# Kernel optimization log

Hardware: AMD Instinct MI355X
Metric: run time of the kernel (lower is better)

The kernel has to match this reference:

```python
import jax, jax.numpy as jnp
import numpy as np

DT = 0.1
TAU_HP = 12.3  # Tm1 high-pass time constant
TAU_LP = 2.3   # Tm1 low-pass time constant

N_NEURONS = 200_000
N_EDGES = 6_400_000
N_TM1 = 25_000
STEPS = 50


def setup_inputs() -> dict:
    key = jax.random.key(0)
    k1, k2, k3, k4 = jax.random.split(key, 4)
    tm1_input = jax.random.normal(k1, (STEPS, N_TM1), dtype=jnp.float32)
    weights = jax.random.normal(k2, (N_EDGES,), dtype=jnp.float32) * 0.1
    tau = jnp.ones((N_NEURONS,), dtype=jnp.float32)      # tau_init = 1.0 per type
    vrest = jnp.zeros((N_NEURONS,), dtype=jnp.float32)   # vrest_init = 0.0 per type
    source_idx = jax.random.randint(k3, (N_EDGES,), 0, N_NEURONS, dtype=jnp.int32)
    target_idx = jax.random.randint(k4, (N_EDGES,), 0, N_NEURONS, dtype=jnp.int32)
    return {
        "tm1_input": tm1_input,
        "weights": weights,
        "tau": tau,
        "vrest": vrest,
        "source_idx": source_idx,
        "target_idx": target_idx,
        "n_tm1": N_TM1,
    }


def reference(tm1_input, weights, tau, vrest, source_idx, target_idx, n_tm1):
    n_neurons = tau.shape[0]

    def step(carry, x):
        v, tm1_f, tm1_v = carry
        # Tm1 temporal filters: high-pass then rectify then low-pass
        hp_out = x - tm1_f                                   # [n_tm1]
        tm1_f_new = tm1_f + DT * (x - tm1_f) / TAU_HP
        rect_out = jax.nn.relu(hp_out)
        # write (old) tm1_v into the Tm1 slice of v before recurrence
        v = v.at[:n_tm1].set(tm1_v)
        tm1_v_new = tm1_v + DT * (rect_out - tm1_v) / TAU_LP
        # gather -> weight -> scatter-add message passing
        r = jax.nn.relu(v)                                   # [n_neurons]
        edge_currents = r[source_idx] * weights              # [n_edges]
        synaptic_input = jax.ops.segment_sum(
            edge_currents, target_idx, num_segments=n_neurons)
        external = jnp.zeros_like(v).at[:n_tm1].set(tm1_v_new)
        dv = (-v + synaptic_input + vrest + external) / tau
        dv = dv.at[:n_tm1].set(0.0)                          # Tm1 driven by its filters
        v = v + DT * dv
        return (v, tm1_f_new, tm1_v_new), None

    v0 = jnp.zeros((tau.shape[0],), dtype=tm1_input.dtype)
    f0 = jnp.zeros((n_tm1,), dtype=tm1_input.dtype)
    tv0 = jnp.zeros((n_tm1,), dtype=tm1_input.dtype)
    (v, _, _), _ = jax.lax.scan(step, (v0, f0, tv0), tm1_input)
    return v[None, :]  # [1, n_neurons], matches torch batch=1
```

## Files before the change

kernel.cpp:

```cpp
#include <hip/hip_runtime.h>
#include <hip/hip_bf16.h>

#define DT 0.1f
#define TAU_HP 12.3f
#define TAU_LP 2.3f
#define SCAN_B 1024

#define BSHIFT 7
#define BMASK 127
#define BMAX 2048
#define CHUNK 32768
#define B4_CAP 6144
#define MWMAX 6400


__global__ void init_kernel(float* __restrict__ vA,
                            float* __restrict__ tm1_f,
                            unsigned* __restrict__ mask3,
                            int n_neurons, int n_tm1, int mask3_words) {
    int i = blockIdx.x * blockDim.x + threadIdx.x;
    if (i < n_neurons) vA[i] = 0.0f;
    if (i < n_tm1) tm1_f[i] = 0.0f;
    if (i < mask3_words) mask3[i] = 0u;
}

__global__ void bhist_kernel(const int* __restrict__ tgt, int* __restrict__ blkhist,
                             int n_edges, int n_tm1, int nb, int nblk) {
    __shared__ int hist[BMAX];
    int b = blockIdx.x;
    for (int i = threadIdx.x; i < nb; i += blockDim.x) hist[i] = 0;
    __syncthreads();
    int base = b * CHUNK;
    int end = min(base + CHUNK, n_edges);
    for (int k = base + threadIdx.x; k < end; k += blockDim.x) {
        int t = tgt[k];
        if (t >= n_tm1) atomicAdd(&hist[t >> BSHIFT], 1);
    }
    __syncthreads();
    for (int i = threadIdx.x; i < nb; i += blockDim.x)
        blkhist[(size_t)i * nblk + b] = hist[i];
}

__global__ void scan1_kernel(const int* in, int* out, int* bsums, int n) {
    __shared__ int s[SCAN_B];
    int gid = blockIdx.x * SCAN_B + threadIdx.x;
    int x = (gid < n) ? in[gid] : 0;
    s[threadIdx.x] = x;
    __syncthreads();
    for (int off = 1; off < SCAN_B; off <<= 1) {
        int t = (threadIdx.x >= off) ? s[threadIdx.x - off] : 0;
        __syncthreads();
        s[threadIdx.x] += t;
        __syncthreads();
    }
    if (gid < n) out[gid] = s[threadIdx.x] - x;
    if (threadIdx.x == SCAN_B - 1) bsums[blockIdx.x] = s[SCAN_B - 1];
}

__global__ void scan2_kernel(int* bsums, int nb, int* total) {
    __shared__ int s[SCAN_B];
    int x = (threadIdx.x < nb) ? bsums[threadIdx.x] : 0;
    s[threadIdx.x] = x;
    __syncthreads();
    for (int off = 1; off < SCAN_B; off <<= 1) {
        int t = (threadIdx.x >= off) ? s[threadIdx.x - off] : 0;
        __syncthreads();
        s[threadIdx.x] += t;
        __syncthreads();
    }
    if (threadIdx.x == nb - 1) *total = s[threadIdx.x];
    if (threadIdx.x < nb) bsums[threadIdx.x] = s[threadIdx.x] - x;
}

__global__ void scanadd_kernel(int* data, const int* __restrict__ bsums, int n) {
    int gid = blockIdx.x * blockDim.x + threadIdx.x;
    if (gid < n) data[gid] += bsums[gid / SCAN_B];
}

__global__ void bin_kernel(const int* __restrict__ src, const int* __restrict__ tgt,
                           const float* __restrict__ w, const int* __restrict__ scanned,
                           int2* __restrict__ edges, int n_edges, int n_tm1,
                           int nb, int nblk) {
    __shared__ int cur[BMAX];
    int b = blockIdx.x;
    for (int i = threadIdx.x; i < nb; i += blockDim.x)
        cur[i] = scanned[(size_t)i * nblk + b];
    __syncthreads();
    int base = b * CHUNK;
    int end = min(base + CHUNK, n_edges);
    for (int k = base + threadIdx.x; k < end; k += blockDim.x) {
        int t = tgt[k];
        if (t < n_tm1) continue;
        int pos = atomicAdd(&cur[t >> BSHIFT], 1);
        edges[pos] = make_int2(src[k] | ((t & BMASK) << 18), __float_as_int(w[k]));
    }
}

__global__ void finalize_kernel(int2* edges, const int* __restrict__ scanned,
                                int* __restrict__ row_start,
                                const int* __restrict__ total,
                                int n_neurons, int nb, int nblk) {
    __shared__ int2 buf[B4_CAP];
    __shared__ int hist[BMASK + 1], ls[BMASK + 1], cur[BMASK + 1];
    int b = blockIdx.x;
    int n_kept = *total;
    int beg = scanned[(size_t)b * nblk];
    int end = (b == nb - 1) ? n_kept : scanned[(size_t)(b + 1) * nblk];
    int n = min(end - beg, B4_CAP);

    for (int k = threadIdx.x; k < n; k += blockDim.x) buf[k] = edges[beg + k];
    if (threadIdx.x <= BMASK) hist[threadIdx.x] = 0;
    __syncthreads();
    for (int k = threadIdx.x; k < n; k += blockDim.x)
        atomicAdd(&hist[(buf[k].x >> 18) & BMASK], 1);
    __syncthreads();
    if (threadIdx.x <= BMASK) ls[threadIdx.x] = hist[threadIdx.x];
    __syncthreads();
    for (int off = 1; off <= BMASK; off <<= 1) {
        int t = (threadIdx.x <= BMASK && threadIdx.x >= off) ? ls[threadIdx.x - off] : 0;
        __syncthreads();
        if (threadIdx.x <= BMASK) ls[threadIdx.x] += t;
        __syncthreads();
    }
    if (threadIdx.x <= BMASK) {
        int excl = ls[threadIdx.x] - hist[threadIdx.x];
        cur[threadIdx.x] = excl;
        int t = (b << BSHIFT) + threadIdx.x;
        if (t < n_neurons) row_start[t] = beg + excl;
    }
    if (b == nb - 1 && threadIdx.x == 0) row_start[n_neurons] = n_kept;
    __syncthreads();
    for (int k = threadIdx.x; k < n; k += blockDim.x) {
        int2 r = buf[k];
        int pos = atomicAdd(&cur[(r.x >> 18) & BMASK], 1);
        edges[beg + pos] = make_int2(r.x & 0x3FFFF, r.y);
    }
}

__global__ __launch_bounds__(1024)
void step_kernel(const int* __restrict__ row_start,
                 const int2* __restrict__ edges,
                 const float* __restrict__ vr,
                 float* __restrict__ vw,
                 float* __restrict__ tm1_f,
                 const float* __restrict__ x,
                 const float* __restrict__ tau,
                 const float* __restrict__ vrest,
                 const unsigned* __restrict__ maskR,
                 unsigned* __restrict__ maskW,
                 unsigned* __restrict__ maskC,
                 int mask_words,
                 int n_neurons, int n_tm1, int gbase, int last) {
    __shared__ unsigned smask[MWMAX];
    int g = blockIdx.x * blockDim.x + threadIdx.x;

    if ((int)((blockIdx.x + 1) * blockDim.x) > gbase) {
        for (int i = threadIdx.x; i < mask_words; i += blockDim.x)
            smask[i] = maskR[i];
        __syncthreads();
    }

    if (g < gbase) {
        if (g < mask_words) maskC[g] = 0u;
        float val = 0.0f;
        bool wrote = false;
        if (g < n_tm1) {
            float cur = vr[g];
            if (last) {
                val = cur;
            } else {
                float f  = tm1_f[g];
                float xk = x[g];
                float hp = xk - f;
                tm1_f[g] = f + DT * (xk - f) / TAU_HP;
                val = cur + DT * (fmaxf(hp, 0.0f) - cur) / TAU_LP;
            }
            vw[g] = val;
            wrote = true;
        }
        unsigned long long bm = __ballot(wrote && (val > 0.0f));
        int l = threadIdx.x & 63;
        unsigned lo = (unsigned)(bm & 0xffffffffull);
        unsigned hi = (unsigned)(bm >> 32);
        if (l == 0 && lo)  atomicOr(&maskW[g >> 5], lo);
        if (l == 32 && hi) atomicOr(&maskW[g >> 5], hi);
        return;
    }

    int t = g - gbase;
    int row = n_tm1 + (t >> 3);
    int lane = t & 7;
    bool active = (row < n_neurons);
    float sum = 0.0f;
    float vnew = 0.0f;

    if (active) {
        int s = row_start[row];
        int e = row_start[row + 1];
        for (int p = (s & ~1) + 2 * lane; p < e; p += 16) {
            int4 q = *(const int4*)(edges + p);
            bool a0 = (p >= s)    && ((smask[(unsigned)q.x >> 5] >> (q.x & 31)) & 1u);
            bool a1 = (p + 1 < e) && ((smask[(unsigned)q.z >> 5] >> (q.z & 31)) & 1u);
            if (a0) sum += vr[q.x] * __int_as_float(q.y);
            if (a1) sum += vr[q.z] * __int_as_float(q.w);
        }
    }
    sum += __shfl_xor(sum, 4);
    sum += __shfl_xor(sum, 2);
    sum += __shfl_xor(sum, 1);
    if (active && lane == 0) {
        float vi = vr[row];
        vnew = vi + DT * ((-vi + sum + vrest[row]) / tau[row]);
        vw[row] = vnew;
    }
    unsigned long long bm = __ballot(active && lane == 0 && vnew > 0.0f);
    if ((threadIdx.x & 63) == 0) {
        unsigned b8 = 0;
        #pragma unroll
        for (int i = 0; i < 8; ++i) b8 |= (unsigned)((bm >> (8 * i)) & 1ull) << i;
        if (b8) {
            int row0 = n_tm1 + (t >> 3);
            atomicOr(&maskW[row0 >> 5], b8 << (row0 & 31));
        }
    }
}

extern "C" void kernel_launch(void* const* d_in, const int* in_sizes, int n_in,
                              void* d_out, int out_size, void* d_ws, size_t ws_size,
                              hipStream_t stream) {
    const float* tm1_input  = (const float*)d_in[0];
    const float* weights    = (const float*)d_in[1];
    const float* tau        = (const float*)d_in[2];
    const float* vrest      = (const float*)d_in[3];
    const int*   source_idx = (const int*)d_in[4];
    const int*   target_idx = (const int*)d_in[5];

    const int n_edges   = in_sizes[1];
    const int n_neurons = in_sizes[2];
    const int n_tm1     = 25000;
    const int steps     = in_sizes[0] / n_tm1;

    const int nb   = (n_neurons + BMASK) >> BSHIFT;
    const int nblk = (n_edges + CHUNK - 1) / CHUNK;
    const int n_scan = nb * nblk;
    const int mask_words = (n_neurons + 31) >> 5;

    size_t off = 0;
    auto alloc = [&](size_t n) { size_t o = off; off += n; return o; };
    int* ws_i = (int*)d_ws;
    float* ws_f = (float*)d_ws;

    int2*     edges     = (int2*)(ws_i + alloc((size_t)(n_edges + 2) * 2));
    float*    vA        = ws_f + alloc(n_neurons);
    float*    vB        = ws_f + alloc(n_neurons);
    float*    tm1_f     = ws_f + alloc(n_tm1);
    int*      row_start = ws_i + alloc(n_neurons + 1);
    unsigned* mask3     = (unsigned*)(ws_i + alloc((size_t)3 * mask_words));
    int*      blkhist   = ws_i + alloc((size_t)n_scan);
    int*      bsums     = ws_i + alloc(SCAN_B);
    int*      total     = ws_i + alloc(1);
    (void)ws_size;

    float* out = (float*)d_out;

    const int B = 256;
    const int gridN = (n_neurons + B - 1) / B;
    const int nScanBlocks = (n_scan + SCAN_B - 1) / SCAN_B;
    const int gridSA = (n_scan + B - 1) / B;

    const int SB = 1024;
    const int gbase = (n_tm1 + 63) & ~63;
    const int work  = gbase + (n_neurons - n_tm1) * 8;
    const int gridG = (work + SB - 1) / SB;

    init_kernel<<<gridN, B, 0, stream>>>(vA, tm1_f, mask3, n_neurons, n_tm1,
                                         3 * mask_words);
    bhist_kernel<<<nblk, 1024, 0, stream>>>(target_idx, blkhist, n_edges, n_tm1,
                                            nb, nblk);
    scan1_kernel<<<nScanBlocks, SCAN_B, 0, stream>>>(blkhist, blkhist, bsums, n_scan);
    scan2_kernel<<<1, SCAN_B, 0, stream>>>(bsums, nScanBlocks, total);
    scanadd_kernel<<<gridSA, B, 0, stream>>>(blkhist, bsums, n_scan);
    bin_kernel<<<nblk, 1024, 0, stream>>>(source_idx, target_idx, weights, blkhist,
                                          edges, n_edges, n_tm1, nb, nblk);
    finalize_kernel<<<nb, 1024, 0, stream>>>(edges, blkhist, row_start, total,
                                             n_neurons, nb, nblk);

    for (int k = 0; k < steps; ++k) {
        const float* vr = (k & 1) ? vB : vA;
        float* vw = (k == steps - 1) ? out : ((k & 1) ? vA : vB);
        unsigned* mW = mask3 + (size_t)(k % 3) * mask_words;
        unsigned* mR = mask3 + (size_t)((k + 2) % 3) * mask_words;
        unsigned* mC = mask3 + (size_t)((k + 1) % 3) * mask_words;
        step_kernel<<<gridG, SB, 0, stream>>>(
            row_start, edges, vr, vw, tm1_f,
            tm1_input + (size_t)k * n_tm1,
            tau, vrest, mR, mW, mC, mask_words,
            n_neurons, n_tm1, gbase, (k == steps - 1) ? 1 : 0);
    }
}
```

Baseline: 1.779 ms.

## Build CSR with global per-target histogram and atomic scatter

Replaces the two-level bucketed CSR build (block histograms, bucket scatter, then an in-shared-memory per-bucket sort) with a direct global atomic histogram over target neurons, a scan, and a global atomic scatter into per-row cursors. This drops the blkhist matrix and the finalize pass, cutting preprocessing kernels and memory traffic. In exchange it relies on contended global atomics and scattered writes. Edge order within a row becomes nondeterministic, so the floating-point summation order varies between runs.

```diff
diff --git a/kernel.cpp b/kernel.cpp
--- a/kernel.cpp
+++ b/kernel.cpp
@@ -5,40 +5,28 @@
 #define TAU_HP 12.3f
 #define TAU_LP 2.3f
 #define SCAN_B 1024
-
-#define BSHIFT 7
-#define BMASK 127
-#define BMAX 2048
-#define CHUNK 32768
-#define B4_CAP 6144
 #define MWMAX 6400
 
 
 __global__ void init_kernel(float* __restrict__ vA,
                             float* __restrict__ tm1_f,
                             unsigned* __restrict__ mask3,
+                            int* __restrict__ row_start,
                             int n_neurons, int n_tm1, int mask3_words) {
     int i = blockIdx.x * blockDim.x + threadIdx.x;
     if (i < n_neurons) vA[i] = 0.0f;
     if (i < n_tm1) tm1_f[i] = 0.0f;
     if (i < mask3_words) mask3[i] = 0u;
-}
-
-__global__ void bhist_kernel(const int* __restrict__ tgt, int* __restrict__ blkhist,
-                             int n_edges, int n_tm1, int nb, int nblk) {
-    __shared__ int hist[BMAX];
-    int b = blockIdx.x;
-    for (int i = threadIdx.x; i < nb; i += blockDim.x) hist[i] = 0;
-    __syncthreads();
-    int base = b * CHUNK;
-    int end = min(base + CHUNK, n_edges);
-    for (int k = base + threadIdx.x; k < end; k += blockDim.x) {
-        int t = tgt[k];
-        if (t >= n_tm1) atomicAdd(&hist[t >> BSHIFT], 1);
-    }
-    __syncthreads();
-    for (int i = threadIdx.x; i < nb; i += blockDim.x)
-        blkhist[(size_t)i * nblk + b] = hist[i];
+    if (i <= n_neurons) row_start[i] = 0;
+}
+
+__global__ void ghist_kernel(const int* __restrict__ tgt, int* __restrict__ hist,
+                             int n_edges, int n_tm1) {
+    int stride = gridDim.x * blockDim.x;
+    for (int i = blockIdx.x * blockDim.x + threadIdx.x; i < n_edges; i += stride) {
+        int t = tgt[i];
+        if (t >= n_tm1) atomicAdd(&hist[t], 1);
+    }
 }
 
 __global__ void scan1_kernel(const int* in, int* out, int* bsums, int n) {
@@ -77,63 +65,27 @@
     if (gid < n) data[gid] += bsums[gid / SCAN_B];
 }
 
-__global__ void bin_kernel(const int* __restrict__ src, const int* __restrict__ tgt,
-                           const float* __restrict__ w, const int* __restrict__ scanned,
-                           int2* __restrict__ edges, int n_edges, int n_tm1,
-                           int nb, int nblk) {
-    __shared__ int cur[BMAX];
-    int b = blockIdx.x;
-    for (int i = threadIdx.x; i < nb; i += blockDim.x)
-        cur[i] = scanned[(size_t)i * nblk + b];
-    __syncthreads();
-    int base = b * CHUNK;
-    int end = min(base + CHUNK, n_edges);
-    for (int k = base + threadIdx.x; k < end; k += blockDim.x) {
-        int t = tgt[k];
+__global__ void mkcur_kernel(const int* __restrict__ row_start,
+                             int* __restrict__ cur,
+                             int* __restrict__ rs_tail,
+                             const int* __restrict__ total, int n_neurons) {
+    int i = blockIdx.x * blockDim.x + threadIdx.x;
+    if (i < n_neurons) cur[i] = row_start[i];
+    if (i == 0) *rs_tail = *total;
+}
+
+__global__ void scatter_kernel(const int* __restrict__ src,
+                               const int* __restrict__ tgt,
+                               const float* __restrict__ w,
+                               int* __restrict__ cur,
+                               int2* __restrict__ edges,
+                               int n_edges, int n_tm1) {
+    int stride = gridDim.x * blockDim.x;
+    for (int i = blockIdx.x * blockDim.x + threadIdx.x; i < n_edges; i += stride) {
+        int t = tgt[i];
         if (t < n_tm1) continue;
-        int pos = atomicAdd(&cur[t >> BSHIFT], 1);
-        edges[pos] = make_int2(src[k] | ((t & BMASK) << 18), __float_as_int(w[k]));
-    }
-}
-
-__global__ void finalize_kernel(int2* edges, const int* __restrict__ scanned,
-                                int* __restrict__ row_start,
-                                const int* __restrict__ total,
-                                int n_neurons, int nb, int nblk) {
-    __shared__ int2 buf[B4_CAP];
-    __shared__ int hist[BMASK + 1], ls[BMASK + 1], cur[BMASK + 1];
-    int b = blockIdx.x;
-    int n_kept = *total;
-    int beg = scanned[(size_t)b * nblk];
-    int end = (b == nb - 1) ? n_kept : scanned[(size_t)(b + 1) * nblk];
-    int n = min(end - beg, B4_CAP);
-
-    for (int k = threadIdx.x; k < n; k += blockDim.x) buf[k] = edges[beg + k];
-    if (threadIdx.x <= BMASK) hist[threadIdx.x] = 0;
-    __syncthreads();
-    for (int k = threadIdx.x; k < n; k += blockDim.x)
-        atomicAdd(&hist[(buf[k].x >> 18) & BMASK], 1);
-    __syncthreads();
-    if (threadIdx.x <= BMASK) ls[threadIdx.x] = hist[threadIdx.x];
-    __syncthreads();
-    for (int off = 1; off <= BMASK; off <<= 1) {
-        int t = (threadIdx.x <= BMASK && threadIdx.x >= off) ? ls[threadIdx.x - off] : 0;
-        __syncthreads();
-        if (threadIdx.x <= BMASK) ls[threadIdx.x] += t;
-        __syncthreads();
-    }
-    if (threadIdx.x <= BMASK) {
-        int excl = ls[threadIdx.x] - hist[threadIdx.x];
-        cur[threadIdx.x] = excl;
-        int t = (b << BSHIFT) + threadIdx.x;
-        if (t < n_neurons) row_start[t] = beg + excl;
-    }
-    if (b == nb - 1 && threadIdx.x == 0) row_start[n_neurons] = n_kept;
-    __syncthreads();
-    for (int k = threadIdx.x; k < n; k += blockDim.x) {
-        int2 r = buf[k];
-        int pos = atomicAdd(&cur[(r.x >> 18) & BMASK], 1);
-        edges[beg + pos] = make_int2(r.x & 0x3FFFF, r.y);
+        int pos = atomicAdd(&cur[t], 1);
+        edges[pos] = make_int2(src[i], __float_as_int(w[i]));
     }
 }
 
@@ -240,9 +192,6 @@
     const int n_tm1     = 25000;
     const int steps     = in_sizes[0] / n_tm1;
 
-    const int nb   = (n_neurons + BMASK) >> BSHIFT;
-    const int nblk = (n_edges + CHUNK - 1) / CHUNK;
-    const int n_scan = nb * nblk;
     const int mask_words = (n_neurons + 31) >> 5;
 
     size_t off = 0;
@@ -255,8 +204,8 @@
     float*    vB        = ws_f + alloc(n_neurons);
     float*    tm1_f     = ws_f + alloc(n_tm1);
     int*      row_start = ws_i + alloc(n_neurons + 1);
+    int*      cur       = ws_i + alloc(n_neurons);
     unsigned* mask3     = (unsigned*)(ws_i + alloc((size_t)3 * mask_words));
-    int*      blkhist   = ws_i + alloc((size_t)n_scan);
     int*      bsums     = ws_i + alloc(SCAN_B);
     int*      total     = ws_i + alloc(1);
     (void)ws_size;
@@ -264,26 +213,27 @@
     float* out = (float*)d_out;
 
     const int B = 256;
-    const int gridN = (n_neurons + B - 1) / B;
-    const int nScanBlocks = (n_scan + SCAN_B - 1) / SCAN_B;
-    const int gridSA = (n_scan + B - 1) / B;
+    const int gridN = (n_neurons + 1 + B - 1) / B;
+    const int nScanBlocks = (n_neurons + SCAN_B - 1) / SCAN_B;
+    const int gridSA = (n_neurons + B - 1) / B;
+    const int gridE = 2048;
 
     const int SB = 1024;
     const int gbase = (n_tm1 + 63) & ~63;
     const int work  = gbase + (n_neurons - n_tm1) * 8;
     const int gridG = (work + SB - 1) / SB;
 
-    init_kernel<<<gridN, B, 0, stream>>>(vA, tm1_f, mask3, n_neurons, n_tm1,
-                                         3 * mask_words);
-    bhist_kernel<<<nblk, 1024, 0, stream>>>(target_idx, blkhist, n_edges, n_tm1,
-                                            nb, nblk);
-    scan1_kernel<<<nScanBlocks, SCAN_B, 0, stream>>>(blkhist, blkhist, bsums, n_scan);
+    init_kernel<<<gridN, B, 0, stream>>>(vA, tm1_f, mask3, row_start,
+                                         n_neurons, n_tm1, 3 * mask_words);
+    ghist_kernel<<<gridE, B, 0, stream>>>(target_idx, row_start, n_edges, n_tm1);
+    scan1_kernel<<<nScanBlocks, SCAN_B, 0, stream>>>(row_start, row_start, bsums,
+                                                     n_neurons);
     scan2_kernel<<<1, SCAN_B, 0, stream>>>(bsums, nScanBlocks, total);
-    scanadd_kernel<<<gridSA, B, 0, stream>>>(blkhist, bsums, n_scan);
-    bin_kernel<<<nblk, 1024, 0, stream>>>(source_idx, target_idx, weights, blkhist,
-                                          edges, n_edges, n_tm1, nb, nblk);
-    finalize_kernel<<<nb, 1024, 0, stream>>>(edges, blkhist, row_start, total,
-                                             n_neurons, nb, nblk);
+    scanadd_kernel<<<gridSA, B, 0, stream>>>(row_start, bsums, n_neurons);
+    mkcur_kernel<<<gridSA, B, 0, stream>>>(row_start, cur, row_start + n_neurons,
+                                           total, n_neurons);
+    scatter_kernel<<<gridE, B, 0, stream>>>(source_idx, target_idx, weights,
+                                            cur, edges, n_edges, n_tm1);
 
     for (int k = 0; k < steps; ++k) {
         const float* vr = (k & 1) ? vB : vA;
```

New measurement: 2.124 ms. 19.4% more time.
